# Performance work log

Hardware: AMD Instinct MI355X
Metric: run time of the kernel (lower is better)

Reference implementation:

```python
import jax, jax.numpy as jnp
import numpy as np

B, T, V, E, H, K = 128, 512, 50257, 100, 128, 12
START, STOP = 10, 11


def setup_inputs() -> dict:
    key = jax.random.key(0)
    ks = jax.random.split(key, 11)
    sentences = jax.random.randint(ks[0], (B, T), 0, V)
    h0 = jax.random.normal(ks[1], (B, H), jnp.float32)
    c0 = jax.random.normal(ks[2], (B, H), jnp.float32)
    embed = jax.random.normal(ks[3], (V, E), jnp.float32) * 0.1
    Wih = jax.random.normal(ks[4], (4 * H, E), jnp.float32) * 0.1   # torch gate order i,f,g,o
    Whh = jax.random.normal(ks[5], (4 * H, H), jnp.float32) * 0.1
    bih = jax.random.normal(ks[6], (4 * H,), jnp.float32) * 0.1
    bhh = jax.random.normal(ks[7], (4 * H,), jnp.float32) * 0.1
    Wtag = jax.random.normal(ks[8], (K, H), jnp.float32) * 0.1
    btag = jax.random.normal(ks[9], (K,), jnp.float32) * 0.1
    transitions = jax.random.normal(ks[10], (K, K), jnp.float32)
    transitions = transitions.at[START, :].set(-10000.0).at[:, STOP].set(-10000.0)
    return dict(sentences=sentences, h0=h0, c0=c0, embed=embed,
                Wih=Wih, Whh=Whh, bih=bih, bhh=bhh,
                Wtag=Wtag, btag=btag, transitions=transitions)


def reference(sentences, h0, c0, embed, Wih, Whh, bih, bhh, Wtag, btag, transitions):
    # --- embedding + single-layer LSTM (batch_first); dropout is identity at eval ---
    x = embed[sentences]                       # [B, T, E]
    x_t = jnp.swapaxes(x, 0, 1)                # [T, B, E]

    def lstm_step(carry, xt):
        h, c = carry
        gates = xt @ Wih.T + h @ Whh.T + bih + bhh      # [B, 4H]
        i, f, g, o = jnp.split(gates, 4, axis=-1)
        c = jax.nn.sigmoid(f) * c + jax.nn.sigmoid(i) * jnp.tanh(g)
        h = jax.nn.sigmoid(o) * jnp.tanh(c)
        return (h, c), h

    _, hs = jax.lax.scan(lstm_step, (h0, c0), x_t)      # hs: [T, B, H]
    emissions = hs @ Wtag.T + btag                      # [T, B, K]

    # --- batched Viterbi DP over time ---
    def vit_step(prev, emit):
        # prev: [B, K] trellis at t-1; transitions[i, j] = score(i -> j)
        v = prev[:, :, None] + transitions[None]        # [B, K, K]
        best = jnp.max(v, axis=1)                       # [B, K]
        bp = jnp.argmax(v, axis=1).astype(jnp.int32)    # [B, K]
        return emit + best, bp

    last, bps = jax.lax.scan(vit_step, emissions[0], emissions[1:])  # bps: [T-1, B, K]
    scores = jnp.max(last, axis=-1)                     # [B]
    last_tag = jnp.argmax(last, axis=-1).astype(jnp.int32)  # [B]

    # --- backtrace (reverse scan) ---
    def back_step(tag, bp):
        prev = jnp.take_along_axis(bp, tag[:, None], axis=1)[:, 0]
        return prev, prev

    _, early_tags = jax.lax.scan(back_step, last_tag, bps, reverse=True)  # [T-1, B]
    paths = jnp.concatenate([early_tags, last_tag[None]], axis=0)         # [T, B]
    paths = jnp.swapaxes(paths, 0, 1)                                     # [B, T]
    return scores, paths
```

## Files before the change

### kernel.cpp

```cpp
#include <hip/hip_runtime.h>
#include <hip/hip_bf16.h>

#define BB 128
#define TT 512
#define EE 100
#define HH 128
#define KK 12
#define VV 50257
#define NB 8
#define NBLK 16

typedef short bf16x8 __attribute__((ext_vector_type(8)));
typedef float f32x4  __attribute__((ext_vector_type(4)));

__device__ __forceinline__ unsigned short f2bf(float x) {
  __hip_bfloat16 h = __float2bfloat16(x);
  return *reinterpret_cast<unsigned short*>(&h);
}
__device__ __forceinline__ float bf2f(unsigned short u) {
  return __uint_as_float(((unsigned)u) << 16);
}

__device__ __forceinline__ bf16x8 load8_bf(const float* p) {
  float4 a = *reinterpret_cast<const float4*>(p);
  float4 b = *reinterpret_cast<const float4*>(p + 4);
  bf16x8 r;
  r[0] = (short)f2bf(a.x); r[1] = (short)f2bf(a.y);
  r[2] = (short)f2bf(a.z); r[3] = (short)f2bf(a.w);
  r[4] = (short)f2bf(b.x); r[5] = (short)f2bf(b.y);
  r[6] = (short)f2bf(b.z); r[7] = (short)f2bf(b.w);
  return r;
}

__device__ __forceinline__ bf16x8 load8_bf_pad_bias(const float* row, int k0,
                                                    float bias) {
  bf16x8 r;
  #pragma unroll
  for (int i = 0; i < 8; ++i) {
    int k = k0 + i;
    unsigned short v = 0;
    if (k < EE) v = f2bf(row[k]);
    else if (k == EE) v = f2bf(bias);
    r[i] = (short)v;
  }
  return r;
}

__device__ __forceinline__ float sigr(float x) {
  float e = __builtin_amdgcn_exp2f(x * -1.44269504f);
  return __builtin_amdgcn_rcpf(1.0f + e);
}
__device__ __forceinline__ float tanhr(float x) {
  float e = __builtin_amdgcn_exp2f(x * -2.88539008f);
  return __fmaf_rn(2.0f, __builtin_amdgcn_rcpf(1.0f + e), -1.0f);
}

__device__ __forceinline__ int frag_idx(int b, int k) {
  return ((k >> 5) << 9) + ((b + (((k >> 3) & 3) << 4)) << 3) + (k & 7);
}

__global__ __launch_bounds__(256) void precast_kernel(
    const float* __restrict__ embed, unsigned short* __restrict__ ebf)
{
  int id = blockIdx.x * 256 + threadIdx.x;
  if (id >= VV * 16) return;
  int v = id >> 4, g = id & 15;
  const float* row = embed + (size_t)v * EE;
  bf16x8 o;
  #pragma unroll
  for (int i = 0; i < 8; ++i) {
    int k = g * 8 + i;
    unsigned short u = 0;
    if (k < EE) u = f2bf(row[k]);
    else if (k == EE) u = 0x3F80;
    o[i] = (short)u;
  }
  *reinterpret_cast<bf16x8*>(ebf + (size_t)id * 8) = o;
}

__global__ __launch_bounds__(256) void wprep_kernel(
    const float* __restrict__ Wih, const float* __restrict__ bih,
    const float* __restrict__ bhh, unsigned short* __restrict__ wbf)
{
  int id = blockIdx.x * 256 + threadIdx.x;
  if (id >= 8 * 4 * 4 * 64) return;
  int l = id & 63, kt = (id >> 6) & 3, tt = (id >> 8) & 3, s8 = id >> 10;
  int gcol = tt * HH + 16 * s8 + (l & 15);
  int k0 = kt * 32 + (l >> 4) * 8;
  float bias = bih[gcol] + bhh[gcol];
  bf16x8 r = load8_bf_pad_bias(Wih + (size_t)gcol * EE, k0, bias);
  *reinterpret_cast<bf16x8*>(wbf + (size_t)id * 8) = r;
}

__global__ __launch_bounds__(256, 2) void pregates_kernel(
    const int* __restrict__ sent, const unsigned short* __restrict__ ebf,
    const unsigned short* __restrict__ wbf, unsigned short* __restrict__ P16)
{
  const int w = threadIdx.x >> 6, l = threadIdx.x & 63;
  const int c = l & 15, q = l >> 4;
  const int rt = blockIdx.x * 4 + w;
  const int flat = rt * 16 + c;
  const int b = flat >> 9, t = flat & 511;
  const int id = sent[b * TT + t];

  bf16x8 xa[4];
  #pragma unroll
  for (int kt = 0; kt < 4; ++kt)
    xa[kt] = *reinterpret_cast<const bf16x8*>(
        ebf + (size_t)id * 128 + kt * 32 + q * 8);

  const bf16x8* wb = reinterpret_cast<const bf16x8*>(wbf);
  #pragma unroll
  for (int s8 = 0; s8 < 8; ++s8) {
    f32x4 acc[4];
    #pragma unroll
    for (int tt = 0; tt < 4; ++tt) {
      f32x4 z = {0.f, 0.f, 0.f, 0.f};
      acc[tt] = z;
    }
    #pragma unroll
    for (int kt = 0; kt < 4; ++kt) {
      #pragma unroll
      for (int tt = 0; tt < 4; ++tt)
        acc[tt] = __builtin_amdgcn_mfma_f32_16x16x32_bf16(
            xa[kt], wb[((s8 * 4 + tt) * 4 + kt) * 64 + l], acc[tt], 0, 0, 0);
    }
    const int e = s8 * 16 + c;
    #pragma unroll
    for (int r4 = 0; r4 < 4; ++r4) {
      int fr = rt * 16 + q * 4 + r4;
      ushort4 o = make_ushort4(f2bf(acc[0][r4]), f2bf(acc[1][r4]),
                               f2bf(acc[2][r4]), f2bf(acc[3][r4]));
      *reinterpret_cast<ushort4*>(P16 + ((size_t)fr * 128 + e) * 4) = o;
    }
  }
}

__global__ __launch_bounds__(512, 2) void lstm_crf_fused(
    const unsigned short* __restrict__ P16, const float* __restrict__ Whh,
    const float* __restrict__ h0, const float* __restrict__ c0,
    const float* __restrict__ Wtag, const float* __restrict__ btag,
    const float* __restrict__ trans, float* __restrict__ out)
{
  __shared__ unsigned char bp[256 * (NB * 12)];
  __shared__ __align__(16) unsigned short hfrag[2][2048];
  __shared__ __align__(16) float vit[NB * 16];
  __shared__ __align__(16) float trl[KK * 16];
  __shared__ __align__(16) float ering[2][NB * 16];
  extern __shared__ char dynpad[];
  (void)dynpad;

  const int bg  = blockIdx.x;
  const int tid = threadIdx.x;
  const int w   = tid >> 6;
  const int l   = tid & 63;
  const int c   = l & 15;
  const int q   = l >> 4;
  const int ew  = 16 * w + c;

  bf16x8 wh[4][4];
  #pragma unroll
  for (int tt = 0; tt < 4; ++tt) {
    const int gcol = tt * HH + ew;
    #pragma unroll
    for (int kt = 0; kt < 4; ++kt)
      wh[tt][kt] = load8_bf(Whh + (size_t)gcol * HH + kt * 32 + q * 8);
  }

  float cst[2];
  #pragma unroll
  for (int r = 0; r < 2; ++r)
    cst[r] = c0[(size_t)(bg * NB + q * 2 + r) * HH + ew];

  bf16x8 we[4];
  #pragma unroll
  for (int kt = 0; kt < 4; ++kt) {
    #pragma unroll
    for (int i = 0; i < 8; ++i) we[kt][i] = 0;
  }
  float bt = 0.f;
  if (w == 0 && c < KK) {
    #pragma unroll
    for (int kt = 0; kt < 4; ++kt)
      we[kt] = load8_bf(Wtag + (size_t)c * HH + kt * 32 + q * 8);
    bt = btag[c];
  }

  {
    int4 z = {0, 0, 0, 0};
    reinterpret_cast<int4*>(hfrag)[tid] = z;
  }
  if (tid < KK * KK) {
    int i = tid / KK, jj = tid - i * KK;
    trl[jj * 16 + i] = trans[tid];
  }
  __syncthreads();

  for (int idx = tid; idx < NB * HH; idx += 512) {
    int lb = idx >> 7, k = idx & 127;
    int row = ((lb >> 1) << 2) + (lb & 1);
    hfrag[0][frag_idx(row, k)] = f2bf(h0[(size_t)(bg * NB + lb) * HH + k]);
  }

  const unsigned short* pb0 =
      P16 + (size_t)(bg * NB + q * 2 + 0) * (TT * 512) + ew * 4;
  const unsigned short* pb1 =
      P16 + (size_t)(bg * NB + q * 2 + 1) * (TT * 512) + ew * 4;
  ushort4 pA[2], pB[2];
  pA[0] = *reinterpret_cast<const ushort4*>(pb0);
  pA[1] = *reinterpret_cast<const ushort4*>(pb1);
  pB[0] = *reinterpret_cast<const ushort4*>(pb0 + 512);
  pB[1] = *reinterpret_cast<const ushort4*>(pb1 + 512);

  const int hw_off = frag_idx(q * 4, ew);
  int nib = 0;
  __syncthreads();

  auto step = [&](int s, ushort4 (&pcur)[2]) {
    const int rb = s & 1;

    bf16x8 ha[4];
    if (s <= TT) {
      const bf16x8* hr = reinterpret_cast<const bf16x8*>(&hfrag[rb][0]) + l;
      #pragma unroll
      for (int kt = 0; kt < 4; ++kt) ha[kt] = hr[kt * 64];
    }

    if (s < TT) {
      f32x4 acc[4];
      #pragma unroll
      for (int tt = 0; tt < 4; ++tt) {
        f32x4 z = {0.f, 0.f, 0.f, 0.f};
        acc[tt] = z;
      }
      acc[0][0] = bf2f(pcur[0].x); acc[1][0] = bf2f(pcur[0].y);
      acc[2][0] = bf2f(pcur[0].z); acc[3][0] = bf2f(pcur[0].w);
      acc[0][1] = bf2f(pcur[1].x); acc[1][1] = bf2f(pcur[1].y);
      acc[2][1] = bf2f(pcur[1].z); acc[3][1] = bf2f(pcur[1].w);

      if (s + 2 < TT) {
        pcur[0] = *reinterpret_cast<const ushort4*>(pb0 + (size_t)(s + 2) * 512);
        pcur[1] = *reinterpret_cast<const ushort4*>(pb1 + (size_t)(s + 2) * 512);
      }

      #pragma unroll
      for (int kt = 0; kt < 4; ++kt) {
        #pragma unroll
        for (int tt = 0; tt < 4; ++tt)
          acc[tt] = __builtin_amdgcn_mfma_f32_16x16x32_bf16(ha[kt], wh[tt][kt], acc[tt], 0, 0, 0);
      }

      unsigned short* hwp = &hfrag[rb ^ 1][hw_off];
      #pragma unroll
      for (int r = 0; r < 2; ++r) {
        float si = sigr(acc[0][r]);
        float sf = sigr(acc[1][r]);
        float tg = tanhr(acc[2][r]);
        float so = sigr(acc[3][r]);
        cst[r] = __fmaf_rn(sf, cst[r], si * tg);
        hwp[r * 8] = f2bf(so * tanhr(cst[r]));
      }
    } else if (s + 2 < TT) {
    }

    if (w == 0 && s >= 1 && s <= TT) {
      f32x4 accE = {0.f, 0.f, 0.f, 0.f};
      #pragma unroll
      for (int kt = 0; kt < 4; ++kt)
        accE = __builtin_amdgcn_mfma_f32_16x16x32_bf16(ha[kt], we[kt], accE, 0, 0, 0);
      float* er = &ering[(s - 1) & 1][0];
      #pragma unroll
      for (int r = 0; r < 2; ++r)
        er[(q * 2 + r) * 16 + c] = accE[r] + bt;
    }

    if (w >= 4 && s >= 2 && q < 2 && c < KK) {
      const int t_ = s - 2;
      const int b = (w - 4) * 2 + q;
      float Ev = ering[t_ & 1][b * 16 + c];
      float nv;
      if (t_ == 0) {
        nv = Ev;
      } else {
        float4 v0 = *reinterpret_cast<const float4*>(&vit[b * 16]);
        float4 v1 = *reinterpret_cast<const float4*>(&vit[b * 16 + 4]);
        float4 v2 = *reinterpret_cast<const float4*>(&vit[b * 16 + 8]);
        float4 t0 = *reinterpret_cast<const float4*>(&trl[c * 16]);
        float4 t1 = *reinterpret_cast<const float4*>(&trl[c * 16 + 4]);
        float4 t2 = *reinterpret_cast<const float4*>(&trl[c * 16 + 8]);
        float cand[KK] = {v0.x + t0.x, v0.y + t0.y, v0.z + t0.z, v0.w + t0.w,
                          v1.x + t1.x, v1.y + t1.y, v1.z + t1.z, v1.w + t1.w,
                          v2.x + t2.x, v2.y + t2.y, v2.z + t2.z, v2.w + t2.w};
        float g0 = fmaxf(fmaxf(cand[0], cand[1]), cand[2]);
        float g1 = fmaxf(fmaxf(cand[3], cand[4]), cand[5]);
        float g2 = fmaxf(fmaxf(cand[6], cand[7]), cand[8]);
        float g3 = fmaxf(fmaxf(cand[9], cand[10]), cand[11]);
        float best = fmaxf(fmaxf(g0, g1), fmaxf(g2, g3));
        int bi = 11;
        #pragma unroll
        for (int i = 10; i >= 0; --i) bi = (cand[i] == best) ? i : bi;
        nv = Ev + best;
        if (t_ & 1) bp[(t_ >> 1) * (NB * 12) + b * 12 + c] =
                        (unsigned char)(nib | (bi << 4));
        else        nib = bi;
      }
      vit[b * 16 + c] = nv;
    }

    __syncthreads();
  };

  for (int s = 0; s < TT + 2; s += 2) {
    step(s, pA);
    step(s + 1, pB);
  }

  unsigned char* pb = reinterpret_cast<unsigned char*>(hfrag);
  if (tid < NB) {
    int b = tid;
    float best = vit[b * 16];
    int tag = 0;
    for (int jj = 1; jj < KK; ++jj) {
      float v = vit[b * 16 + jj];
      if (v > best) { best = v; tag = jj; }
    }
    out[bg * NB + b] = best;
    pb[b * 512 + 511] = (unsigned char)tag;
    for (int t_ = TT - 1; t_ >= 1; --t_) {
      unsigned char byte = bp[(t_ >> 1) * (NB * 12) + b * 12 + tag];
      tag = (t_ & 1) ? (byte >> 4) & 15 : (byte & 15);
      pb[b * 512 + t_ - 1] = (unsigned char)tag;
    }
  }
  __syncthreads();

  #pragma unroll
  for (int i = 0; i < NB; ++i) {
    int idx = tid + i * 512;
    out[BB + (size_t)(bg * NB + (idx >> 9)) * TT + (idx & 511)] = (float)pb[idx];
  }
}

extern "C" void kernel_launch(void* const* d_in, const int* in_sizes, int n_in,
                              void* d_out, int out_size, void* d_ws, size_t ws_size,
                              hipStream_t stream) {
  const int*   sent  = (const int*)d_in[0];
  const float* h0    = (const float*)d_in[1];
  const float* c0    = (const float*)d_in[2];
  const float* embed = (const float*)d_in[3];
  const float* Wih   = (const float*)d_in[4];
  const float* Whh   = (const float*)d_in[5];
  const float* bih   = (const float*)d_in[6];
  const float* bhh   = (const float*)d_in[7];
  const float* Wtag  = (const float*)d_in[8];
  const float* btag  = (const float*)d_in[9];
  const float* trans = (const float*)d_in[10];
  float* out = (float*)d_out;

  unsigned short* ebf = (unsigned short*)d_ws;
  unsigned short* wbf = ebf + (size_t)VV * 128;
  unsigned short* P16 = wbf + 8192 * 8;

  precast_kernel<<<(VV * 16 + 255) / 256, 256, 0, stream>>>(embed, ebf);
  wprep_kernel<<<32, 256, 0, stream>>>(Wih, bih, bhh, wbf);
  pregates_kernel<<<(BB * TT / 16) / 4, 256, 0, stream>>>(sent, ebf, wbf, P16);
  lstm_crf_fused<<<NBLK, 512, 56 * 1024, stream>>>(
      P16, Whh, h0, c0, Wtag, btag, trans, out);
}
```

Baseline: 536.1 us.

## Halve batch per block to 4 and double LSTM-CRF blocks, fuse gate math

Reduces the batch rows handled per workgroup from 8 to 4 and doubles the grid to 32 blocks, so each lane processes one batch row instead of two. This cuts the serial per-step gate work on the recurrent critical path and spreads the scan across more CUs. The activation math is also fused: the sigmoid-times-tanh products share one reciprocal each, and the cell state is clamped before its tanh. The cost is that half of each MFMA tile's rows now carry no useful work, and the same Whh weights are loaded into twice as many blocks.

```diff
diff --git a/kernel.cpp b/kernel.cpp
--- a/kernel.cpp
+++ b/kernel.cpp
@@ -7,8 +7,8 @@
 #define HH 128
 #define KK 12
 #define VV 50257
-#define NB 8
-#define NBLK 16
+#define NB 4
+#define NBLK 32
 
 typedef short bf16x8 __attribute__((ext_vector_type(8)));
 typedef float f32x4  __attribute__((ext_vector_type(4)));
@@ -44,15 +44,6 @@
     r[i] = (short)v;
   }
   return r;
-}
-
-__device__ __forceinline__ float sigr(float x) {
-  float e = __builtin_amdgcn_exp2f(x * -1.44269504f);
-  return __builtin_amdgcn_rcpf(1.0f + e);
-}
-__device__ __forceinline__ float tanhr(float x) {
-  float e = __builtin_amdgcn_exp2f(x * -2.88539008f);
-  return __fmaf_rn(2.0f, __builtin_amdgcn_rcpf(1.0f + e), -1.0f);
 }
 
 __device__ __forceinline__ int frag_idx(int b, int k) {
@@ -167,10 +158,7 @@
       wh[tt][kt] = load8_bf(Whh + (size_t)gcol * HH + kt * 32 + q * 8);
   }
 
-  float cst[2];
-  #pragma unroll
-  for (int r = 0; r < 2; ++r)
-    cst[r] = c0[(size_t)(bg * NB + q * 2 + r) * HH + ew];
+  float cst = c0[(size_t)(bg * NB + q) * HH + ew];
 
   bf16x8 we[4];
   #pragma unroll
@@ -196,27 +184,21 @@
   }
   __syncthreads();
 
-  for (int idx = tid; idx < NB * HH; idx += 512) {
-    int lb = idx >> 7, k = idx & 127;
-    int row = ((lb >> 1) << 2) + (lb & 1);
-    hfrag[0][frag_idx(row, k)] = f2bf(h0[(size_t)(bg * NB + lb) * HH + k]);
+  if (tid < NB * HH) {
+    int lb = tid >> 7, k = tid & 127;
+    hfrag[0][frag_idx(lb * 4, k)] = f2bf(h0[(size_t)(bg * NB + lb) * HH + k]);
   }
 
   const unsigned short* pb0 =
-      P16 + (size_t)(bg * NB + q * 2 + 0) * (TT * 512) + ew * 4;
-  const unsigned short* pb1 =
-      P16 + (size_t)(bg * NB + q * 2 + 1) * (TT * 512) + ew * 4;
-  ushort4 pA[2], pB[2];
-  pA[0] = *reinterpret_cast<const ushort4*>(pb0);
-  pA[1] = *reinterpret_cast<const ushort4*>(pb1);
-  pB[0] = *reinterpret_cast<const ushort4*>(pb0 + 512);
-  pB[1] = *reinterpret_cast<const ushort4*>(pb1 + 512);
+      P16 + (size_t)(bg * NB + q) * (TT * 512) + ew * 4;
+  ushort4 pA = *reinterpret_cast<const ushort4*>(pb0);
+  ushort4 pB = *reinterpret_cast<const ushort4*>(pb0 + 512);
 
   const int hw_off = frag_idx(q * 4, ew);
   int nib = 0;
   __syncthreads();
 
-  auto step = [&](int s, ushort4 (&pcur)[2]) {
+  auto step = [&](int s, ushort4& pcur) {
     const int rb = s & 1;
 
     bf16x8 ha[4];
@@ -233,15 +215,11 @@
         f32x4 z = {0.f, 0.f, 0.f, 0.f};
         acc[tt] = z;
       }
-      acc[0][0] = bf2f(pcur[0].x); acc[1][0] = bf2f(pcur[0].y);
-      acc[2][0] = bf2f(pcur[0].z); acc[3][0] = bf2f(pcur[0].w);
-      acc[0][1] = bf2f(pcur[1].x); acc[1][1] = bf2f(pcur[1].y);
-      acc[2][1] = bf2f(pcur[1].z); acc[3][1] = bf2f(pcur[1].w);
-
-      if (s + 2 < TT) {
-        pcur[0] = *reinterpret_cast<const ushort4*>(pb0 + (size_t)(s + 2) * 512);
-        pcur[1] = *reinterpret_cast<const ushort4*>(pb1 + (size_t)(s + 2) * 512);
-      }
+      acc[0][0] = bf2f(pcur.x); acc[1][0] = bf2f(pcur.y);
+      acc[2][0] = bf2f(pcur.z); acc[3][0] = bf2f(pcur.w);
+
+      if (s + 2 < TT)
+        pcur = *reinterpret_cast<const ushort4*>(pb0 + (size_t)(s + 2) * 512);
 
       #pragma unroll
       for (int kt = 0; kt < 4; ++kt) {
@@ -250,17 +228,17 @@
           acc[tt] = __builtin_amdgcn_mfma_f32_16x16x32_bf16(ha[kt], wh[tt][kt], acc[tt], 0, 0, 0);
       }
 
-      unsigned short* hwp = &hfrag[rb ^ 1][hw_off];
-      #pragma unroll
-      for (int r = 0; r < 2; ++r) {
-        float si = sigr(acc[0][r]);
-        float sf = sigr(acc[1][r]);
-        float tg = tanhr(acc[2][r]);
-        float so = sigr(acc[3][r]);
-        cst[r] = __fmaf_rn(sf, cst[r], si * tg);
-        hwp[r * 8] = f2bf(so * tanhr(cst[r]));
-      }
-    } else if (s + 2 < TT) {
+      float ai = __builtin_amdgcn_exp2f(acc[0][0] * -1.44269504f);
+      float bg_ = __builtin_amdgcn_exp2f(acc[2][0] * -2.88539008f);
+      float af = __builtin_amdgcn_exp2f(acc[1][0] * -1.44269504f);
+      float ao = __builtin_amdgcn_exp2f(acc[3][0] * -1.44269504f);
+      float sitg = (1.0f - bg_) * __builtin_amdgcn_rcpf((1.0f + ai) * (1.0f + bg_));
+      float sf = __builtin_amdgcn_rcpf(1.0f + af);
+      cst = __fmaf_rn(sf, cst, sitg);
+      float cc = fminf(fmaxf(cst, -30.0f), 30.0f);
+      float ec = __builtin_amdgcn_exp2f(cc * -2.88539008f);
+      float hv = (1.0f - ec) * __builtin_amdgcn_rcpf((1.0f + ao) * (1.0f + ec));
+      hfrag[rb ^ 1][hw_off] = f2bf(hv);
     }
 
     if (w == 0 && s >= 1 && s <= TT) {
@@ -268,15 +246,12 @@
       #pragma unroll
       for (int kt = 0; kt < 4; ++kt)
         accE = __builtin_amdgcn_mfma_f32_16x16x32_bf16(ha[kt], we[kt], accE, 0, 0, 0);
-      float* er = &ering[(s - 1) & 1][0];
-      #pragma unroll
-      for (int r = 0; r < 2; ++r)
-        er[(q * 2 + r) * 16 + c] = accE[r] + bt;
-    }
-
-    if (w >= 4 && s >= 2 && q < 2 && c < KK) {
+      ering[(s - 1) & 1][q * 16 + c] = accE[0] + bt;
+    }
+
+    if (w >= 4 && s >= 2 && q == 0 && c < KK) {
       const int t_ = s - 2;
-      const int b = (w - 4) * 2 + q;
+      const int b = w - 4;
       float Ev = ering[t_ & 1][b * 16 + c];
       float nv;
       if (t_ == 0) {
@@ -364,6 +339,6 @@
   precast_kernel<<<(VV * 16 + 255) / 256, 256, 0, stream>>>(embed, ebf);
   wprep_kernel<<<32, 256, 0, stream>>>(Wih, bih, bhh, wbf);
   pregates_kernel<<<(BB * TT / 16) / 4, 256, 0, stream>>>(sent, ebf, wbf, P16);
-  lstm_crf_fused<<<NBLK, 512, 56 * 1024, stream>>>(
+  lstm_crf_fused<<<NBLK, 512, 60 * 1024, stream>>>(
       P16, Whh, h0, c0, Wtag, btag, trans, out);
 }
```

Measured after the change: 689.1 us. +28.5%, slower.

## Split fused LSTM-CRF into LSTM, emission GEMM and per-sentence Viterbi kernels

Applied to the files above, without the earlier changes.

The fused recurrent kernel, which ran emission MFMA and Viterbi DP inside each LSTM step on 16 blocks, becomes three kernels. The LSTM writes bf16 hidden states to a workspace, a separate batched MFMA kernel computes emissions, and a Viterbi kernel runs one block per sentence across 128 blocks. The gate math is also merged so sigmoid(i)*tanh(g) and sigmoid(o)*tanh(c) each need one reciprocal, and an LDS padding array is kept to hold occupancy. The aim is a shorter LSTM critical path per step and more parallel Viterbi. The cost is extra global traffic for hidden states and emissions, two more launches, and a serial Viterbi that now runs after the LSTM instead of overlapping it.

```diff
diff --git a/kernel.cpp b/kernel.cpp
--- a/kernel.cpp
+++ b/kernel.cpp
@@ -46,15 +46,6 @@
   return r;
 }
 
-__device__ __forceinline__ float sigr(float x) {
-  float e = __builtin_amdgcn_exp2f(x * -1.44269504f);
-  return __builtin_amdgcn_rcpf(1.0f + e);
-}
-__device__ __forceinline__ float tanhr(float x) {
-  float e = __builtin_amdgcn_exp2f(x * -2.88539008f);
-  return __fmaf_rn(2.0f, __builtin_amdgcn_rcpf(1.0f + e), -1.0f);
-}
-
 __device__ __forceinline__ int frag_idx(int b, int k) {
   return ((k >> 5) << 9) + ((b + (((k >> 3) & 3) << 4)) << 3) + (k & 7);
 }
@@ -136,19 +127,13 @@
   }
 }
 
-__global__ __launch_bounds__(512, 2) void lstm_crf_fused(
+__global__ __launch_bounds__(512, 2) void lstm_kernel(
     const unsigned short* __restrict__ P16, const float* __restrict__ Whh,
     const float* __restrict__ h0, const float* __restrict__ c0,
-    const float* __restrict__ Wtag, const float* __restrict__ btag,
-    const float* __restrict__ trans, float* __restrict__ out)
-{
-  __shared__ unsigned char bp[256 * (NB * 12)];
+    unsigned short* __restrict__ hst)
+{
   __shared__ __align__(16) unsigned short hfrag[2][2048];
-  __shared__ __align__(16) float vit[NB * 16];
-  __shared__ __align__(16) float trl[KK * 16];
-  __shared__ __align__(16) float ering[2][NB * 16];
-  extern __shared__ char dynpad[];
-  (void)dynpad;
+  __shared__ __align__(16) unsigned int lpad[7168];
 
   const int bg  = blockIdx.x;
   const int tid = threadIdx.x;
@@ -172,28 +157,13 @@
   for (int r = 0; r < 2; ++r)
     cst[r] = c0[(size_t)(bg * NB + q * 2 + r) * HH + ew];
 
-  bf16x8 we[4];
-  #pragma unroll
-  for (int kt = 0; kt < 4; ++kt) {
-    #pragma unroll
-    for (int i = 0; i < 8; ++i) we[kt][i] = 0;
-  }
-  float bt = 0.f;
-  if (w == 0 && c < KK) {
-    #pragma unroll
-    for (int kt = 0; kt < 4; ++kt)
-      we[kt] = load8_bf(Wtag + (size_t)c * HH + kt * 32 + q * 8);
-    bt = btag[c];
-  }
-
   {
     int4 z = {0, 0, 0, 0};
     reinterpret_cast<int4*>(hfrag)[tid] = z;
   }
-  if (tid < KK * KK) {
-    int i = tid / KK, jj = tid - i * KK;
-    trl[jj * 16 + i] = trans[tid];
-  }
+  for (int i = tid; i < 7168; i += 512) lpad[i] = 0u;
+  unsigned int keep = lpad[tid];
+  asm volatile("" :: "v"(keep));
   __syncthreads();
 
   for (int idx = tid; idx < NB * HH; idx += 512) {
@@ -212,21 +182,27 @@
   pB[0] = *reinterpret_cast<const ushort4*>(pb0 + 512);
   pB[1] = *reinterpret_cast<const ushort4*>(pb1 + 512);
 
+  unsigned short hp[2] = {0, 0};
+  unsigned short* hb0 = hst + (size_t)(bg * NB + q * 2 + 0) * TT * HH + ew;
+  unsigned short* hb1 = hst + (size_t)(bg * NB + q * 2 + 1) * TT * HH + ew;
+
   const int hw_off = frag_idx(q * 4, ew);
-  int nib = 0;
   __syncthreads();
 
   auto step = [&](int s, ushort4 (&pcur)[2]) {
     const int rb = s & 1;
 
-    bf16x8 ha[4];
-    if (s <= TT) {
+    if (s >= 1 && s <= TT) {
+      hb0[(size_t)(s - 1) * HH] = hp[0];
+      hb1[(size_t)(s - 1) * HH] = hp[1];
+    }
+
+    if (s < TT) {
+      bf16x8 ha[4];
       const bf16x8* hr = reinterpret_cast<const bf16x8*>(&hfrag[rb][0]) + l;
       #pragma unroll
       for (int kt = 0; kt < 4; ++kt) ha[kt] = hr[kt * 64];
-    }
-
-    if (s < TT) {
+
       f32x4 acc[4];
       #pragma unroll
       for (int tt = 0; tt < 4; ++tt) {
@@ -253,60 +229,23 @@
       unsigned short* hwp = &hfrag[rb ^ 1][hw_off];
       #pragma unroll
       for (int r = 0; r < 2; ++r) {
-        float si = sigr(acc[0][r]);
-        float sf = sigr(acc[1][r]);
-        float tg = tanhr(acc[2][r]);
-        float so = sigr(acc[3][r]);
-        cst[r] = __fmaf_rn(sf, cst[r], si * tg);
-        hwp[r * 8] = f2bf(so * tanhr(cst[r]));
+        float ai  = __builtin_amdgcn_exp2f(acc[0][r] * -1.44269504f);
+        float bgg = __builtin_amdgcn_exp2f(acc[2][r] * -2.88539008f);
+        float af  = __builtin_amdgcn_exp2f(acc[1][r] * -1.44269504f);
+        float ao  = __builtin_amdgcn_exp2f(acc[3][r] * -1.44269504f);
+        float sitg = (1.0f - bgg) *
+                     __builtin_amdgcn_rcpf((1.0f + ai) * (1.0f + bgg));
+        float sf = __builtin_amdgcn_rcpf(1.0f + af);
+        cst[r] = __fmaf_rn(sf, cst[r], sitg);
+        float cc = fminf(fmaxf(cst[r], -30.0f), 30.0f);
+        float ec = __builtin_amdgcn_exp2f(cc * -2.88539008f);
+        float hv = (1.0f - ec) *
+                   __builtin_amdgcn_rcpf((1.0f + ao) * (1.0f + ec));
+        unsigned short hu = f2bf(hv);
+        hwp[r * 8] = hu;
+        hp[r] = hu;
       }
-    } else if (s + 2 < TT) {
-    }
-
-    if (w == 0 && s >= 1 && s <= TT) {
-      f32x4 accE = {0.f, 0.f, 0.f, 0.f};
-      #pragma unroll
-      for (int kt = 0; kt < 4; ++kt)
-        accE = __builtin_amdgcn_mfma_f32_16x16x32_bf16(ha[kt], we[kt], accE, 0, 0, 0);
-      float* er = &ering[(s - 1) & 1][0];
-      #pragma unroll
-      for (int r = 0; r < 2; ++r)
-        er[(q * 2 + r) * 16 + c] = accE[r] + bt;
-    }
-
-    if (w >= 4 && s >= 2 && q < 2 && c < KK) {
-      const int t_ = s - 2;
-      const int b = (w - 4) * 2 + q;
-      float Ev = ering[t_ & 1][b * 16 + c];
-      float nv;
-      if (t_ == 0) {
-        nv = Ev;
-      } else {
-        float4 v0 = *reinterpret_cast<const float4*>(&vit[b * 16]);
-        float4 v1 = *reinterpret_cast<const float4*>(&vit[b * 16 + 4]);
-        float4 v2 = *reinterpret_cast<const float4*>(&vit[b * 16 + 8]);
-        float4 t0 = *reinterpret_cast<const float4*>(&trl[c * 16]);
-        float4 t1 = *reinterpret_cast<const float4*>(&trl[c * 16 + 4]);
-        float4 t2 = *reinterpret_cast<const float4*>(&trl[c * 16 + 8]);
-        float cand[KK] = {v0.x + t0.x, v0.y + t0.y, v0.z + t0.z, v0.w + t0.w,
-                          v1.x + t1.x, v1.y + t1.y, v1.z + t1.z, v1.w + t1.w,
-                          v2.x + t2.x, v2.y + t2.y, v2.z + t2.z, v2.w + t2.w};
-        float g0 = fmaxf(fmaxf(cand[0], cand[1]), cand[2]);
-        float g1 = fmaxf(fmaxf(cand[3], cand[4]), cand[5]);
-        float g2 = fmaxf(fmaxf(cand[6], cand[7]), cand[8]);
-        float g3 = fmaxf(fmaxf(cand[9], cand[10]), cand[11]);
-        float best = fmaxf(fmaxf(g0, g1), fmaxf(g2, g3));
-        int bi = 11;
-        #pragma unroll
-        for (int i = 10; i >= 0; --i) bi = (cand[i] == best) ? i : bi;
-        nv = Ev + best;
-        if (t_ & 1) bp[(t_ >> 1) * (NB * 12) + b * 12 + c] =
-                        (unsigned char)(nib | (bi << 4));
-        else        nib = bi;
-      }
-      vit[b * 16 + c] = nv;
-    }
-
+    }
     __syncthreads();
   };
 
@@ -314,31 +253,130 @@
     step(s, pA);
     step(s + 1, pB);
   }
-
-  unsigned char* pb = reinterpret_cast<unsigned char*>(hfrag);
-  if (tid < NB) {
-    int b = tid;
-    float best = vit[b * 16];
+}
+
+__global__ __launch_bounds__(256, 2) void emis_kernel(
+    const unsigned short* __restrict__ hst, const float* __restrict__ Wtag,
+    const float* __restrict__ btag, float* __restrict__ E)
+{
+  const int w = threadIdx.x >> 6, l = threadIdx.x & 63;
+  const int c = l & 15, q = l >> 4;
+  const int rt = blockIdx.x * 4 + w;
+
+  bf16x8 we[4];
+  #pragma unroll
+  for (int kt = 0; kt < 4; ++kt) {
+    #pragma unroll
+    for (int i = 0; i < 8; ++i) we[kt][i] = 0;
+  }
+  float bt = 0.f;
+  if (c < KK) {
+    #pragma unroll
+    for (int kt = 0; kt < 4; ++kt)
+      we[kt] = load8_bf(Wtag + (size_t)c * HH + kt * 32 + q * 8);
+    bt = btag[c];
+  }
+
+  bf16x8 ha[4];
+  #pragma unroll
+  for (int kt = 0; kt < 4; ++kt)
+    ha[kt] = *reinterpret_cast<const bf16x8*>(
+        hst + (size_t)(rt * 16 + c) * HH + kt * 32 + q * 8);
+
+  f32x4 acc = {0.f, 0.f, 0.f, 0.f};
+  #pragma unroll
+  for (int kt = 0; kt < 4; ++kt)
+    acc = __builtin_amdgcn_mfma_f32_16x16x32_bf16(ha[kt], we[kt], acc, 0, 0, 0);
+
+  #pragma unroll
+  for (int r = 0; r < 4; ++r)
+    E[(size_t)(rt * 16 + q * 4 + r) * 16 + c] = acc[r] + bt;
+}
+
+__global__ __launch_bounds__(64) void vit_kernel(
+    const float* __restrict__ E, const float* __restrict__ trans,
+    float* __restrict__ out)
+{
+  __shared__ __align__(16) float trl[KK * 16];
+  __shared__ __align__(16) float vit[16];
+  __shared__ unsigned char bp[TT * KK];
+  __shared__ unsigned char path[TT];
+
+  const int b = blockIdx.x, tid = threadIdx.x;
+  if (tid < KK * KK) {
+    int i = tid / KK, jj = tid - i * KK;
+    trl[jj * 16 + i] = trans[tid];
+  }
+  __syncthreads();
+
+  const int j = tid;
+  const float* Eb = E + (size_t)b * TT * 16 + j;
+
+  float cur[8], nxt[8];
+  if (j < 16) {
+    #pragma unroll
+    for (int i = 0; i < 8; ++i) cur[i] = Eb[i * 16];
+  }
+
+  for (int tb = 0; tb < TT; tb += 8) {
+    if (j < 16 && tb + 8 < TT) {
+      #pragma unroll
+      for (int i = 0; i < 8; ++i) nxt[i] = Eb[(size_t)(tb + 8 + i) * 16];
+    }
+    #pragma unroll
+    for (int i = 0; i < 8; ++i) {
+      const int t = tb + i;
+      if (j < KK) {
+        float Ev = cur[i];
+        float nv;
+        if (t == 0) {
+          nv = Ev;
+        } else {
+          float4 v0 = *reinterpret_cast<const float4*>(&vit[0]);
+          float4 v1 = *reinterpret_cast<const float4*>(&vit[4]);
+          float4 v2 = *reinterpret_cast<const float4*>(&vit[8]);
+          float4 t0 = *reinterpret_cast<const float4*>(&trl[j * 16]);
+          float4 t1 = *reinterpret_cast<const float4*>(&trl[j * 16 + 4]);
+          float4 t2 = *reinterpret_cast<const float4*>(&trl[j * 16 + 8]);
+          float cand[KK] = {v0.x + t0.x, v0.y + t0.y, v0.z + t0.z, v0.w + t0.w,
+                            v1.x + t1.x, v1.y + t1.y, v1.z + t1.z, v1.w + t1.w,
+                            v2.x + t2.x, v2.y + t2.y, v2.z + t2.z, v2.w + t2.w};
+          float g0 = fmaxf(fmaxf(cand[0], cand[1]), cand[2]);
+          float g1 = fmaxf(fmaxf(cand[3], cand[4]), cand[5]);
+          float g2 = fmaxf(fmaxf(cand[6], cand[7]), cand[8]);
+          float g3 = fmaxf(fmaxf(cand[9], cand[10]), cand[11]);
+          float best = fmaxf(fmaxf(g0, g1), fmaxf(g2, g3));
+          int bi = 11;
+          #pragma unroll
+          for (int k = 10; k >= 0; --k) bi = (cand[k] == best) ? k : bi;
+          nv = Ev + best;
+          bp[t * KK + j] = (unsigned char)bi;
+        }
+        vit[j] = nv;
+      }
+      __syncthreads();
+    }
+    #pragma unroll
+    for (int i = 0; i < 8; ++i) cur[i] = nxt[i];
+  }
+
+  if (tid == 0) {
+    float best = vit[0];
     int tag = 0;
-    for (int jj = 1; jj < KK; ++jj) {
-      float v = vit[b * 16 + jj];
-      if (v > best) { best = v; tag = jj; }
-    }
-    out[bg * NB + b] = best;
-    pb[b * 512 + 511] = (unsigned char)tag;
-    for (int t_ = TT - 1; t_ >= 1; --t_) {
-      unsigned char byte = bp[(t_ >> 1) * (NB * 12) + b * 12 + tag];
-      tag = (t_ & 1) ? (byte >> 4) & 15 : (byte & 15);
-      pb[b * 512 + t_ - 1] = (unsigned char)tag;
+    for (int jj = 1; jj < KK; ++jj)
+      if (vit[jj] > best) { best = vit[jj]; tag = jj; }
+    out[b] = best;
+    path[TT - 1] = (unsigned char)tag;
+    for (int t = TT - 1; t >= 1; --t) {
+      tag = bp[t * KK + tag];
+      path[t - 1] = (unsigned char)tag;
     }
   }
   __syncthreads();
 
   #pragma unroll
-  for (int i = 0; i < NB; ++i) {
-    int idx = tid + i * 512;
-    out[BB + (size_t)(bg * NB + (idx >> 9)) * TT + (idx & 511)] = (float)pb[idx];
-  }
+  for (int i = 0; i < 8; ++i)
+    out[BB + (size_t)b * TT + tid + i * 64] = (float)path[tid + i * 64];
 }
 
 extern "C" void kernel_launch(void* const* d_in, const int* in_sizes, int n_in,
@@ -360,10 +398,13 @@
   unsigned short* ebf = (unsigned short*)d_ws;
   unsigned short* wbf = ebf + (size_t)VV * 128;
   unsigned short* P16 = wbf + 8192 * 8;
+  unsigned short* hst = P16 + (size_t)BB * TT * 512;
+  float*          Ebf = (float*)(hst + (size_t)BB * TT * HH);
 
   precast_kernel<<<(VV * 16 + 255) / 256, 256, 0, stream>>>(embed, ebf);
   wprep_kernel<<<32, 256, 0, stream>>>(Wih, bih, bhh, wbf);
   pregates_kernel<<<(BB * TT / 16) / 4, 256, 0, stream>>>(sent, ebf, wbf, P16);
-  lstm_crf_fused<<<NBLK, 512, 56 * 1024, stream>>>(
-      P16, Whh, h0, c0, Wtag, btag, trans, out);
-}
+  lstm_kernel<<<NBLK, 512, 0, stream>>>(P16, Whh, h0, c0, hst);
+  emis_kernel<<<(BB * TT / 16) / 4, 256, 0, stream>>>(hst, Wtag, btag, Ebf);
+  vit_kernel<<<BB, 64, 0, stream>>>(Ebf, trans, out);
+}
```

Measured after the change: 533.9 us. About the same (-0.4%).
